# Performance work log

Measured on AMD Instinct MI355X. Metric: run time of the kernel, lower is better.

The kernel has to match this reference:

```python
import jax, jax.numpy as jnp
import numpy as np
import math

B, T, D, H, FF = 2, 2048, 1024, 16, 4096
DH = D // H
EPS = 1e-5

def _ternary(key, out_f, in_f):
    # TFLELayer: ternary-quantized linear weight in {-1,0,1} (stored as f32 here)
    return jax.random.randint(key, (out_f, in_f), -1, 2).astype(jnp.float32)

def setup_inputs() -> dict:
    key = jax.random.key(0)
    ks = jax.random.split(key, 8)
    x = jax.random.normal(ks[0], (B, T, D), dtype=jnp.float32)
    mask = jnp.triu(jnp.ones((T, T), dtype=bool), k=1)  # True = masked (causal)
    return {
        "x": x,
        "mask": mask,
        "ln1_g": jnp.ones((D,), jnp.float32), "ln1_b": jnp.zeros((D,), jnp.float32),
        "ln2_g": jnp.ones((D,), jnp.float32), "ln2_b": jnp.zeros((D,), jnp.float32),
        "Wq": _ternary(ks[1], D, D), "Wk": _ternary(ks[2], D, D),
        "Wv": _ternary(ks[3], D, D), "Wo": _ternary(ks[4], D, D),
        "Wff1": _ternary(ks[5], FF, D), "Wff2": _ternary(ks[6], D, FF),
    }

def _ln(x, g, b):
    mu = jnp.mean(x, axis=-1, keepdims=True)
    var = jnp.var(x, axis=-1, keepdims=True)
    return (x - mu) * jax.lax.rsqrt(var + EPS) * g + b

def reference(x, mask, ln1_g, ln1_b, ln2_g, ln2_b, Wq, Wk, Wv, Wo, Wff1, Wff2):
    h = _ln(x, ln1_g, ln1_b)
    q = (h @ Wq.T).reshape(B, T, H, DH).transpose(0, 2, 1, 3)  # (B,H,T,DH)
    k = (h @ Wk.T).reshape(B, T, H, DH).transpose(0, 2, 1, 3)
    v = (h @ Wv.T).reshape(B, T, H, DH).transpose(0, 2, 1, 3)
    scale = 1.0 / math.sqrt(DH)
    attn = jnp.einsum('bhqd,bhkd->bhqk', q, k) * scale
    attn = jnp.where(mask[None, None], -jnp.inf, attn)
    attn = jax.nn.softmax(attn, axis=-1)
    out = jnp.einsum('bhqk,bhkd->bhqd', attn, v)
    out = out.transpose(0, 2, 1, 3).reshape(B, T, D) @ Wo.T
    x = x + out
    h = _ln(x, ln2_g, ln2_b)
    ff = jax.nn.gelu(h @ Wff1.T, approximate=False)
    ff = ff @ Wff2.T
    return x + ff
```

## Files before the change

kernel.cpp:

```cpp
#include <hip/hip_runtime.h>

typedef __bf16 bf16;
typedef bf16 bf16x8 __attribute__((ext_vector_type(8)));
typedef bf16 bf16x4 __attribute__((ext_vector_type(4)));
typedef float f32x4 __attribute__((ext_vector_type(4)));

static __device__ __forceinline__ void async16(const void* g, void* l) {
  __builtin_amdgcn_global_load_lds((__attribute__((address_space(1))) void*)g,
                                   (__attribute__((address_space(3))) void*)l,
                                   16, 0, 0);
}

template <int N>
static __device__ __forceinline__ float ror16(float x) {
  const int y =
      __builtin_amdgcn_update_dpp(0, __float_as_int(x), 0x120 | N, 0xf, 0xf, true);
  return __int_as_float(y);
}
static __device__ __forceinline__ float rowmax16(float x) {
  x = fmaxf(x, ror16<8>(x));
  x = fmaxf(x, ror16<4>(x));
  x = fmaxf(x, ror16<2>(x));
  x = fmaxf(x, ror16<1>(x));
  return x;
}
static __device__ __forceinline__ float rowsum16(float x) {
  x += ror16<8>(x);
  x += ror16<4>(x);
  x += ror16<2>(x);
  x += ror16<1>(x);
  return x;
}

__global__ __launch_bounds__(256) void ln1_cvt4(
    const float* __restrict__ x, const float* __restrict__ g,
    const float* __restrict__ b, bf16* __restrict__ hi, bf16* __restrict__ lo,
    const float* __restrict__ Wq, const float* __restrict__ Wk,
    const float* __restrict__ Wv, const float* __restrict__ Wo,
    bf16* __restrict__ wdst) {
  const int tid = threadIdx.x;
  if (blockIdx.x >= 4096) {
    const size_t i = ((size_t)(blockIdx.x - 4096) * 256 + tid) * 4;
    const size_t M1 = 1u << 20;
    const float* src = (i < M1) ? Wq : (i < 2 * M1) ? Wk : (i < 3 * M1) ? Wv : Wo;
    const size_t off = i & (M1 - 1);
    const float4 v = *(const float4*)(src + off);
    bf16x4 o = {(bf16)v.x, (bf16)v.y, (bf16)v.z, (bf16)v.w};
    *(bf16x4*)(wdst + i) = o;
    return;
  }
  const int row = blockIdx.x;
  const float* xr = x + (size_t)row * 1024;
  float v[4];
  float s1 = 0.f, s2 = 0.f;
#pragma unroll
  for (int j = 0; j < 4; ++j) {
    v[j] = xr[j * 256 + tid];
    s1 += v[j];
    s2 += v[j] * v[j];
  }
#pragma unroll
  for (int off = 1; off < 64; off <<= 1) {
    s1 += __shfl_xor(s1, off);
    s2 += __shfl_xor(s2, off);
  }
  __shared__ float ws1[4], ws2[4];
  const int wid = tid >> 6;
  if ((tid & 63) == 0) {
    ws1[wid] = s1;
    ws2[wid] = s2;
  }
  __syncthreads();
  s1 = ws1[0] + ws1[1] + ws1[2] + ws1[3];
  s2 = ws2[0] + ws2[1] + ws2[2] + ws2[3];
  const float mu = s1 * (1.f / 1024.f);
  const float var = s2 * (1.f / 1024.f) - mu * mu;
  const float rstd = 1.0f / sqrtf(var + 1e-5f);
#pragma unroll
  for (int j = 0; j < 4; ++j) {
    const int cc = j * 256 + tid;
    const float y = (v[j] - mu) * rstd * g[cc] + b[cc];
    const bf16 yh = (bf16)y;
    hi[(size_t)row * 1024 + cc] = yh;
    lo[(size_t)row * 1024 + cc] = (bf16)(y - (float)yh);
  }
}

__global__ __launch_bounds__(256) void ln_kernel(
    const float* __restrict__ x, const float* __restrict__ g,
    const float* __restrict__ b, bf16* __restrict__ hi) {
  const int row = blockIdx.x;
  const int tid = threadIdx.x;
  const float* xr = x + (size_t)row * 1024;
  float v[4];
  float s1 = 0.f, s2 = 0.f;
#pragma unroll
  for (int j = 0; j < 4; ++j) {
    v[j] = xr[j * 256 + tid];
    s1 += v[j];
    s2 += v[j] * v[j];
  }
#pragma unroll
  for (int off = 1; off < 64; off <<= 1) {
    s1 += __shfl_xor(s1, off);
    s2 += __shfl_xor(s2, off);
  }
  __shared__ float ws1[4], ws2[4];
  const int wid = tid >> 6;
  if ((tid & 63) == 0) {
    ws1[wid] = s1;
    ws2[wid] = s2;
  }
  __syncthreads();
  s1 = ws1[0] + ws1[1] + ws1[2] + ws1[3];
  s2 = ws2[0] + ws2[1] + ws2[2] + ws2[3];
  const float mu = s1 * (1.f / 1024.f);
  const float var = s2 * (1.f / 1024.f) - mu * mu;
  const float rstd = 1.0f / sqrtf(var + 1e-5f);
#pragma unroll
  for (int j = 0; j < 4; ++j) {
    const int cc = j * 256 + tid;
    const float y = (v[j] - mu) * rstd * g[cc] + b[cc];
    hi[(size_t)row * 1024 + cc] = (bf16)y;
  }
}

template <int EPI>
static __device__ __forceinline__ void gemm_body(
    const bf16* __restrict__ A, const bf16* __restrict__ B,
    void* __restrict__ Cv, const float* __restrict__ R, bf16* smem, int col0,
    int row0, int M, int N, int K) {
  bf16* sA0 = smem;
  bf16* sA1 = smem + 4096;
  bf16* sB0 = smem + 8192;
  bf16* sB1 = smem + 12288;
  const int tid = threadIdx.x;
  const int lane = tid & 63;
  const int wid = tid >> 6;
  const int wm = wid >> 1, wn = wid & 1;

  f32x4 acc[4][4];
  const f32x4 fzero = {0.f, 0.f, 0.f, 0.f};
#pragma unroll
  for (int i = 0; i < 4; ++i)
#pragma unroll
    for (int j = 0; j < 4; ++j) acc[i][j] = fzero;

  const int nk = K >> 6;
  const int r0 = tid >> 2, c0 = (tid & 3) << 3;
  const int r1 = (256 + tid) >> 2, c1 = ((256 + tid) & 3) << 3;
  const int wofs0 = (wid << 6) * 8;
  const int wofs1 = (256 + (wid << 6)) * 8;

  for (int kt = 0; kt < nk; ++kt) {
    const int k0 = kt << 6;
    async16(A + (size_t)(row0 + r0) * K + k0 + c0, sA0 + wofs0);
    async16(A + (size_t)(row0 + r1) * K + k0 + c1, sA0 + wofs1);
    async16(A + (size_t)(row0 + r0) * K + k0 + 32 + c0, sA1 + wofs0);
    async16(A + (size_t)(row0 + r1) * K + k0 + 32 + c1, sA1 + wofs1);
    async16(B + (size_t)(col0 + r0) * K + k0 + c0, sB0 + wofs0);
    async16(B + (size_t)(col0 + r1) * K + k0 + c1, sB0 + wofs1);
    async16(B + (size_t)(col0 + r0) * K + k0 + 32 + c0, sB1 + wofs0);
    async16(B + (size_t)(col0 + r1) * K + k0 + 32 + c1, sB1 + wofs1);
    __syncthreads();
    const int fr = lane & 15, fq = (lane >> 4) << 3;
#pragma unroll
    for (int t = 0; t < 2; ++t) {
      const bf16* sA = t ? sA1 : sA0;
      const bf16* sB = t ? sB1 : sB0;
      bf16x8 af[4], bfr[4];
#pragma unroll
      for (int i = 0; i < 4; ++i)
        af[i] = *(const bf16x8*)&sA[(wm * 64 + i * 16 + fr) * 32 + fq];
#pragma unroll
      for (int j = 0; j < 4; ++j)
        bfr[j] = *(const bf16x8*)&sB[(wn * 64 + j * 16 + fr) * 32 + fq];
#pragma unroll
      for (int i = 0; i < 4; ++i)
#pragma unroll
        for (int j = 0; j < 4; ++j)
          acc[i][j] = __builtin_amdgcn_mfma_f32_16x16x32_bf16(
              af[i], bfr[j], acc[i][j], 0, 0, 0);
    }
    __syncthreads();
  }

  const int fr = lane & 15, fq4 = (lane >> 4) << 2;
#pragma unroll
  for (int i = 0; i < 4; ++i) {
#pragma unroll
    for (int j = 0; j < 4; ++j) {
      const int rbase = row0 + wm * 64 + i * 16 + fq4;
      const int col = col0 + wn * 64 + j * 16 + fr;
      if constexpr (EPI == 5) {
        const int b = rbase >> 11, t = rbase & 2047;
        const int hh = col >> 6, d = col & 63;
        bf16x4 o4 = {(bf16)acc[i][j][0], (bf16)acc[i][j][1],
                     (bf16)acc[i][j][2], (bf16)acc[i][j][3]};
        *(bf16x4*)&((bf16*)Cv)[(((size_t)(b * 16 + hh)) * 64 + d) * 2048 + t] =
            o4;
      } else {
#pragma unroll
        for (int r = 0; r < 4; ++r) {
          const size_t idx = (size_t)(rbase + r) * N + col;
          const float val = acc[i][j][r];
          if constexpr (EPI == 0) {
            ((float*)Cv)[idx] = val;
          } else if constexpr (EPI == 2) {
            ((float*)Cv)[idx] = val + R[idx];
          } else {
            ((bf16*)Cv)[idx] =
                (bf16)(0.5f * val * (1.0f + erff(val * 0.7071067811865476f)));
          }
        }
      }
    }
  }
}

template <int EPI>
__global__ __launch_bounds__(256) void gemm_bt(
    const bf16* __restrict__ A, const bf16* __restrict__ B,
    void* __restrict__ Cv, const float* __restrict__ R, int M, int N, int K) {
  __shared__ bf16 smem[16384];
  gemm_body<EPI>(A, B, Cv, R, smem, blockIdx.x * 128, blockIdx.y * 128, M, N,
                 K);
}

static __device__ __forceinline__ void gemm_split_merged(
    const bf16* __restrict__ A, const bf16* __restrict__ A2,
    const bf16* __restrict__ B, bf16* __restrict__ Chi, bf16* __restrict__ Clo,
    bf16* smem, float scale, int col0, int row0) {
  constexpr int K = 1024, N = 1024;
  bf16* sAh0 = smem;
  bf16* sAh1 = smem + 4096;
  bf16* sAl0 = smem + 8192;
  bf16* sAl1 = smem + 12288;
  bf16* sB0 = smem + 16384;
  bf16* sB1 = smem + 20480;
  const int tid = threadIdx.x;
  const int lane = tid & 63;
  const int wid = tid >> 6;
  const int wm = wid >> 1, wn = wid & 1;

  f32x4 acc[4][4];
  const f32x4 fzero = {0.f, 0.f, 0.f, 0.f};
#pragma unroll
  for (int i = 0; i < 4; ++i)
#pragma unroll
    for (int j = 0; j < 4; ++j) acc[i][j] = fzero;

  const int r0 = tid >> 2, c0 = (tid & 3) << 3;
  const int r1 = (256 + tid) >> 2, c1 = ((256 + tid) & 3) << 3;
  const int wofs0 = (wid << 6) * 8;
  const int wofs1 = (256 + (wid << 6)) * 8;

  for (int kt = 0; kt < 16; ++kt) {
    const int k0 = kt << 6;
    async16(A + (size_t)(row0 + r0) * K + k0 + c0, sAh0 + wofs0);
    async16(A + (size_t)(row0 + r1) * K + k0 + c1, sAh0 + wofs1);
    async16(A + (size_t)(row0 + r0) * K + k0 + 32 + c0, sAh1 + wofs0);
    async16(A + (size_t)(row0 + r1) * K + k0 + 32 + c1, sAh1 + wofs1);
    async16(A2 + (size_t)(row0 + r0) * K + k0 + c0, sAl0 + wofs0);
    async16(A2 + (size_t)(row0 + r1) * K + k0 + c1, sAl0 + wofs1);
    async16(A2 + (size_t)(row0 + r0) * K + k0 + 32 + c0, sAl1 + wofs0);
    async16(A2 + (size_t)(row0 + r1) * K + k0 + 32 + c1, sAl1 + wofs1);
    async16(B + (size_t)(col0 + r0) * K + k0 + c0, sB0 + wofs0);
    async16(B + (size_t)(col0 + r1) * K + k0 + c1, sB0 + wofs1);
    async16(B + (size_t)(col0 + r0) * K + k0 + 32 + c0, sB1 + wofs0);
    async16(B + (size_t)(col0 + r1) * K + k0 + 32 + c1, sB1 + wofs1);
    __syncthreads();
    const int fr = lane & 15, fq = (lane >> 4) << 3;
#pragma unroll
    for (int t = 0; t < 2; ++t) {
      const bf16* sAh = t ? sAh1 : sAh0;
      const bf16* sAl = t ? sAl1 : sAl0;
      const bf16* sB = t ? sB1 : sB0;
      bf16x8 ah[4], al[4], bfr[4];
#pragma unroll
      for (int i = 0; i < 4; ++i) {
        ah[i] = *(const bf16x8*)&sAh[(wm * 64 + i * 16 + fr) * 32 + fq];
        al[i] = *(const bf16x8*)&sAl[(wm * 64 + i * 16 + fr) * 32 + fq];
      }
#pragma unroll
      for (int j = 0; j < 4; ++j)
        bfr[j] = *(const bf16x8*)&sB[(wn * 64 + j * 16 + fr) * 32 + fq];
#pragma unroll
      for (int i = 0; i < 4; ++i)
#pragma unroll
        for (int j = 0; j < 4; ++j) {
          acc[i][j] = __builtin_amdgcn_mfma_f32_16x16x32_bf16(
              ah[i], bfr[j], acc[i][j], 0, 0, 0);
          acc[i][j] = __builtin_amdgcn_mfma_f32_16x16x32_bf16(
              al[i], bfr[j], acc[i][j], 0, 0, 0);
        }
    }
    __syncthreads();
  }

  const int fr = lane & 15, fq4 = (lane >> 4) << 2;
#pragma unroll
  for (int i = 0; i < 4; ++i)
#pragma unroll
    for (int j = 0; j < 4; ++j) {
      const int rbase = row0 + wm * 64 + i * 16 + fq4;
      const int col = col0 + wn * 64 + j * 16 + fr;
#pragma unroll
      for (int r = 0; r < 4; ++r) {
        const size_t idx = (size_t)(rbase + r) * N + col;
        const float vs = acc[i][j][r] * scale;
        const bf16 hi = (bf16)vs;
        Chi[idx] = hi;
        Clo[idx] = (bf16)(vs - (float)hi);
      }
    }
}

__global__ __launch_bounds__(256) void gemm_qkv(
    const bf16* __restrict__ A, const bf16* __restrict__ A2,
    const bf16* __restrict__ Bq, const bf16* __restrict__ Bk,
    const bf16* __restrict__ Bv, bf16* qh, bf16* ql, bf16* kh, bf16* kl,
    bf16* vt) {
  __shared__ bf16 smem[24576];
  const int which = blockIdx.x >> 3;
  const int col0 = (blockIdx.x & 7) * 128, row0 = blockIdx.y * 128;
  if (which == 2) {
    gemm_body<5>(A, Bv, (void*)vt, nullptr, smem, col0, row0, 4096, 1024,
                 1024);
  } else {
    gemm_split_merged(A, A2, which ? Bk : Bq, which ? kh : qh, which ? kl : ql,
                      smem, which ? 1.0f : 0.125f * 1.44269504088896f, col0,
                      row0);
  }
}

template <int EPI>
__global__ __launch_bounds__(256) void gemm_bt64(
    const bf16* __restrict__ A, const bf16* __restrict__ B,
    void* __restrict__ Cv, const float* __restrict__ R, int M, int N, int K) {
  __shared__ bf16 smem[12288];
  bf16* sA0 = smem;
  bf16* sA1 = smem + 4096;
  bf16* sB0 = smem + 8192;
  bf16* sB1 = smem + 10240;
  const int col0 = blockIdx.x * 64, row0 = blockIdx.y * 128;
  const int tid = threadIdx.x;
  const int lane = tid & 63;
  const int wid = tid >> 6;
  const int wm = wid >> 1, wn = wid & 1;

  f32x4 acc[4][2];
  const f32x4 fzero = {0.f, 0.f, 0.f, 0.f};
#pragma unroll
  for (int i = 0; i < 4; ++i)
#pragma unroll
    for (int j = 0; j < 2; ++j) acc[i][j] = fzero;

  const int nk = K >> 6;
  const int r0 = tid >> 2, c0 = (tid & 3) << 3;
  const int r1 = (256 + tid) >> 2, c1 = ((256 + tid) & 3) << 3;
  const int wofs0 = (wid << 6) * 8;
  const int wofs1 = (256 + (wid << 6)) * 8;

  for (int kt = 0; kt < nk; ++kt) {
    const int k0 = kt << 6;
    async16(A + (size_t)(row0 + r0) * K + k0 + c0, sA0 + wofs0);
    async16(A + (size_t)(row0 + r1) * K + k0 + c1, sA0 + wofs1);
    async16(A + (size_t)(row0 + r0) * K + k0 + 32 + c0, sA1 + wofs0);
    async16(A + (size_t)(row0 + r1) * K + k0 + 32 + c1, sA1 + wofs1);
    async16(B + (size_t)(col0 + r0) * K + k0 + c0, sB0 + wofs0);
    async16(B + (size_t)(col0 + r0) * K + k0 + 32 + c0, sB1 + wofs0);
    __syncthreads();
    const int fr = lane & 15, fq = (lane >> 4) << 3;
#pragma unroll
    for (int t = 0; t < 2; ++t) {
      const bf16* sA = t ? sA1 : sA0;
      const bf16* sB = t ? sB1 : sB0;
      bf16x8 af[4], bfr[2];
#pragma unroll
      for (int i = 0; i < 4; ++i)
        af[i] = *(const bf16x8*)&sA[(wm * 64 + i * 16 + fr) * 32 + fq];
#pragma unroll
      for (int j = 0; j < 2; ++j)
        bfr[j] = *(const bf16x8*)&sB[(wn * 32 + j * 16 + fr) * 32 + fq];
#pragma unroll
      for (int i = 0; i < 4; ++i)
#pragma unroll
        for (int j = 0; j < 2; ++j)
          acc[i][j] = __builtin_amdgcn_mfma_f32_16x16x32_bf16(
              af[i], bfr[j], acc[i][j], 0, 0, 0);
    }
    __syncthreads();
  }

  const int fr = lane & 15, fq4 = (lane >> 4) << 2;
#pragma unroll
  for (int i = 0; i < 4; ++i) {
#pragma unroll
    for (int j = 0; j < 2; ++j) {
      const int rbase = row0 + wm * 64 + i * 16 + fq4;
      const int col = col0 + wn * 32 + j * 16 + fr;
#pragma unroll
      for (int r = 0; r < 4; ++r) {
        const size_t idx = (size_t)(rbase + r) * N + col;
        const float val = acc[i][j][r];
        if constexpr (EPI == 2) {
          ((float*)Cv)[idx] = val + R[idx];
        } else {
          ((float*)Cv)[idx] = val;
        }
      }
    }
  }
}

__global__ __launch_bounds__(256) void attn_cvt2(
    const bf16* __restrict__ qh_g, const bf16* __restrict__ ql_g,
    const bf16* __restrict__ kh_g, const bf16* __restrict__ kl_g,
    const bf16* __restrict__ vt_g, bf16* __restrict__ out,
    const float* __restrict__ Wf1, const float* __restrict__ Wf2,
    bf16* __restrict__ wdst) {
  __shared__ bf16 lds[18688];
  const int tid = threadIdx.x;
  if (blockIdx.x >= 1024) {
    const size_t i = ((size_t)(blockIdx.x - 1024) * 256 + tid) * 4;
    const size_t M4 = 4u << 20;
    const float* src = (i < M4) ? Wf1 : Wf2;
    const size_t off = (i < M4) ? i : i - M4;
    const float4 v = *(const float4*)(src + off);
    bf16x4 o4 = {(bf16)v.x, (bf16)v.y, (bf16)v.z, (bf16)v.w};
    *(bf16x4*)(wdst + i) = o4;
    return;
  }
  bf16* Kh = lds;
  bf16* Kl = lds + 4608;
  bf16* Vt = lds + 9216;
  bf16* Ps = lds + 13824;

  const int bid = blockIdx.x;
  const int qt = 31 - (bid >> 5);
  const int h = bid & 15;
  const int b = (bid >> 4) & 1;
  const int t0 = qt << 6;
  const int w = tid >> 6;
  const int lane = tid & 63;
  const int c = lane & 15;
  const int quad = lane >> 4;

  const int r0 = tid >> 3, c0 = (tid & 7) << 3;
  const int r1 = (tid + 256) >> 3, c1 = ((tid + 256) & 7) << 3;

  const size_t qrow =
      ((size_t)(b * 2048 + t0 + w * 16 + c)) * 1024 + h * 64 + quad * 8;
  bf16x8 aqh[2], aql[2];
  aqh[0] = *(const bf16x8*)&qh_g[qrow];
  aqh[1] = *(const bf16x8*)&qh_g[qrow + 32];
  aql[0] = *(const bf16x8*)&ql_g[qrow];
  aql[1] = *(const bf16x8*)&ql_g[qrow + 32];

  f32x4 o[4];
  const f32x4 fzero = {0.f, 0.f, 0.f, 0.f};
#pragma unroll
  for (int j = 0; j < 4; ++j) o[j] = fzero;
  float m_i[4] = {-3e38f, -3e38f, -3e38f, -3e38f};
  float l_i[4] = {0.f, 0.f, 0.f, 0.f};

  const size_t vtb = ((size_t)(b * 16 + h)) * 64 * 2048;
  const size_t kband = ((size_t)(b * 2048)) * 1024 + h * 64;

  bf16x8 gk[6];
  {
    gk[0] = *(const bf16x8*)&kh_g[kband + (size_t)r0 * 1024 + c0];
    gk[1] = *(const bf16x8*)&kh_g[kband + (size_t)r1 * 1024 + c1];
    gk[2] = *(const bf16x8*)&kl_g[kband + (size_t)r0 * 1024 + c0];
    gk[3] = *(const bf16x8*)&kl_g[kband + (size_t)r1 * 1024 + c1];
    gk[4] = *(const bf16x8*)&vt_g[vtb + (size_t)r0 * 2048 + c0];
    gk[5] = *(const bf16x8*)&vt_g[vtb + (size_t)r1 * 2048 + c1];
  }

  for (int kt = 0; kt <= qt; ++kt) {
    __syncthreads();
    *(bf16x8*)&Kh[r0 * 72 + c0] = gk[0];
    *(bf16x8*)&Kh[r1 * 72 + c1] = gk[1];
    *(bf16x8*)&Kl[r0 * 72 + c0] = gk[2];
    *(bf16x8*)&Kl[r1 * 72 + c1] = gk[3];
    *(bf16x8*)&Vt[r0 * 72 + c0] = gk[4];
    *(bf16x8*)&Vt[r1 * 72 + c1] = gk[5];
    __syncthreads();

    if (kt < qt) {
      const int kb1 = (kt + 1) << 6;
      const size_t kbase = kband + (size_t)kb1 * 1024;
      gk[0] = *(const bf16x8*)&kh_g[kbase + (size_t)r0 * 1024 + c0];
      gk[1] = *(const bf16x8*)&kh_g[kbase + (size_t)r1 * 1024 + c1];
      gk[2] = *(const bf16x8*)&kl_g[kbase + (size_t)r0 * 1024 + c0];
      gk[3] = *(const bf16x8*)&kl_g[kbase + (size_t)r1 * 1024 + c1];
      gk[4] = *(const bf16x8*)&vt_g[vtb + (size_t)r0 * 2048 + kb1 + c0];
      gk[5] = *(const bf16x8*)&vt_g[vtb + (size_t)r1 * 2048 + kb1 + c1];
    }

    bf16x8 bkh[4][2], bkl[4][2];
#pragma unroll
    for (int j = 0; j < 4; ++j)
#pragma unroll
      for (int s = 0; s < 2; ++s) {
        bkh[j][s] = *(const bf16x8*)&Kh[(j * 16 + c) * 72 + s * 32 + quad * 8];
        bkl[j][s] = *(const bf16x8*)&Kl[(j * 16 + c) * 72 + s * 32 + quad * 8];
      }

    f32x4 s4[4];
#pragma unroll
    for (int j = 0; j < 4; ++j) s4[j] = fzero;
#pragma unroll
    for (int j = 0; j < 4; ++j)
#pragma unroll
      for (int s = 0; s < 2; ++s) {
        s4[j] = __builtin_amdgcn_mfma_f32_16x16x32_bf16(aqh[s], bkh[j][s], s4[j], 0, 0, 0);
        s4[j] = __builtin_amdgcn_mfma_f32_16x16x32_bf16(aqh[s], bkl[j][s], s4[j], 0, 0, 0);
        s4[j] = __builtin_amdgcn_mfma_f32_16x16x32_bf16(aql[s], bkh[j][s], s4[j], 0, 0, 0);
      }

    if (kt == qt) {
#pragma unroll
      for (int j = 0; j < 4; ++j)
#pragma unroll
        for (int r = 0; r < 4; ++r)
          if (j * 16 + c > w * 16 + quad * 4 + r) s4[j][r] = -3e38f;
    }

    float al[4], p[4][4];
#pragma unroll
    for (int r = 0; r < 4; ++r) {
      float mt = fmaxf(fmaxf(s4[0][r], s4[1][r]), fmaxf(s4[2][r], s4[3][r]));
      mt = rowmax16(mt);
      const float mn = fmaxf(m_i[r], mt);
      al[r] = exp2f(m_i[r] - mn);
      float ps = 0.f;
#pragma unroll
      for (int j = 0; j < 4; ++j) {
        p[r][j] = exp2f(s4[j][r] - mn);
        ps += p[r][j];
      }
      ps = rowsum16(ps);
      l_i[r] = l_i[r] * al[r] + ps;
      m_i[r] = mn;
#pragma unroll
      for (int j = 0; j < 4; ++j) o[j][r] *= al[r];
    }

    bf16* Pw = Ps + w * 16 * 76;
#pragma unroll
    for (int r = 0; r < 4; ++r)
#pragma unroll
      for (int j = 0; j < 4; ++j)
        Pw[(quad * 4 + r) * 76 + j * 16 + c] = (bf16)p[r][j];

    bf16x8 ap[2], bv[4][2];
#pragma unroll
    for (int s = 0; s < 2; ++s)
      ap[s] = *(const bf16x8*)&Pw[c * 76 + s * 32 + quad * 8];
#pragma unroll
    for (int j = 0; j < 4; ++j)
#pragma unroll
      for (int s = 0; s < 2; ++s)
        bv[j][s] = *(const bf16x8*)&Vt[(j * 16 + c) * 72 + s * 32 + quad * 8];
#pragma unroll
    for (int j = 0; j < 4; ++j)
#pragma unroll
      for (int s = 0; s < 2; ++s)
        o[j] = __builtin_amdgcn_mfma_f32_16x16x32_bf16(ap[s], bv[j][s], o[j], 0, 0, 0);
  }

#pragma unroll
  for (int r = 0; r < 4; ++r) {
    const float inv = 1.0f / l_i[r];
#pragma unroll
    for (int j = 0; j < 4; ++j) {
      const size_t oi =
          ((size_t)(b * 2048 + t0 + w * 16 + quad * 4 + r)) * 1024 + h * 64 +
          j * 16 + c;
      out[oi] = (bf16)(o[j][r] * inv);
    }
  }
}

extern "C" void kernel_launch(void* const* d_in, const int* in_sizes, int n_in,
                              void* d_out, int out_size, void* d_ws,
                              size_t ws_size, hipStream_t stream) {
  const float* x = (const float*)d_in[0];
  const float* g1 = (const float*)d_in[2];
  const float* b1 = (const float*)d_in[3];
  const float* g2 = (const float*)d_in[4];
  const float* b2 = (const float*)d_in[5];
  const float* Wq = (const float*)d_in[6];
  const float* Wk = (const float*)d_in[7];
  const float* Wv = (const float*)d_in[8];
  const float* Wo = (const float*)d_in[9];
  const float* Wf1 = (const float*)d_in[10];
  const float* Wf2 = (const float*)d_in[11];
  char* ws = (char*)d_ws;
  const size_t MB = 1024 * 1024;
  const size_t M1 = 1u << 20;
  bf16* Wq_b = (bf16*)ws;
  bf16* Wk_b = Wq_b + 1 * M1;
  bf16* Wv_b = Wq_b + 2 * M1;
  bf16* Wo_b = Wq_b + 3 * M1;
  bf16* h_hi = (bf16*)(ws + 8 * MB);
  bf16* h_lo = (bf16*)(ws + 16 * MB);
  bf16* Wf1_b = h_hi;
  bf16* Wf2_b = h_lo;
  bf16* qh = (bf16*)(ws + 24 * MB);
  bf16* ql = (bf16*)(ws + 32 * MB);
  bf16* kh = (bf16*)(ws + 40 * MB);
  bf16* kl = (bf16*)(ws + 48 * MB);
  bf16* vt = (bf16*)(ws + 56 * MB);
  bf16* attnout = (bf16*)(ws + 64 * MB);
  float* x1 = (float*)qh;
  bf16* h2 = (bf16*)(ws + 72 * MB);
  bf16* ff = kh;
  float* outp = (float*)d_out;

  ln1_cvt4<<<8192, 256, 0, stream>>>(x, g1, b1, h_hi, h_lo, Wq, Wk, Wv, Wo,
                                     Wq_b);
  gemm_qkv<<<dim3(24, 32), 256, 0, stream>>>(h_hi, h_lo, Wq_b, Wk_b, Wv_b, qh,
                                             ql, kh, kl, vt);
  attn_cvt2<<<9216, 256, 0, stream>>>(qh, ql, kh, kl, vt, attnout, Wf1, Wf2,
                                      Wf1_b);
  gemm_bt64<2><<<dim3(16, 32), 256, 0, stream>>>(attnout, Wo_b, (void*)x1, x,
                                                 4096, 1024, 1024);
  ln_kernel<<<4096, 256, 0, stream>>>(x1, g2, b2, h2);
  gemm_bt<3><<<dim3(32, 32), 256, 0, stream>>>(h2, Wf1_b, (void*)ff, nullptr,
                                               4096, 4096, 1024);
  gemm_bt64<2><<<dim3(16, 32), 256, 0, stream>>>(ff, Wf2_b, (void*)outp, x1,
                                                 4096, 1024, 4096);
}
```

Before: 419.5 us.

## Deepen GEMM K-tile, add lazy softmax rescale and MFMA priority hints

The 64-wide GEMM now loads a 128-deep K slice per iteration into doubled shared memory, which halves the number of barrier pairs per tile. The attention kernel adds s_setprio around its MFMA blocks. It also skips the running-max update and the rescale of the output accumulator when every row's new max exceeds the old one by no more than 8, in log2 units. These cut synchronisation and ALU work in exchange for more LDS use, which may lower occupancy. Lazy rescaling lets exponentials grow up to 2^8, so bf16 P values lose some relative headroom.

After: 422.1 us. Within noise of the previous version (+0.6%).

```diff
diff --git a/kernel.cpp b/kernel.cpp
--- a/kernel.cpp
+++ b/kernel.cpp
@@ -338,11 +338,7 @@
 __global__ __launch_bounds__(256) void gemm_bt64(
     const bf16* __restrict__ A, const bf16* __restrict__ B,
     void* __restrict__ Cv, const float* __restrict__ R, int M, int N, int K) {
-  __shared__ bf16 smem[12288];
-  bf16* sA0 = smem;
-  bf16* sA1 = smem + 4096;
-  bf16* sB0 = smem + 8192;
-  bf16* sB1 = smem + 10240;
+  __shared__ bf16 smem[24576];
   const int col0 = blockIdx.x * 64, row0 = blockIdx.y * 128;
   const int tid = threadIdx.x;
   const int lane = tid & 63;
@@ -356,26 +352,28 @@
 #pragma unroll
     for (int j = 0; j < 2; ++j) acc[i][j] = fzero;
 
-  const int nk = K >> 6;
+  const int nk = K >> 7;
   const int r0 = tid >> 2, c0 = (tid & 3) << 3;
   const int r1 = (256 + tid) >> 2, c1 = ((256 + tid) & 3) << 3;
   const int wofs0 = (wid << 6) * 8;
   const int wofs1 = (256 + (wid << 6)) * 8;
 
   for (int kt = 0; kt < nk; ++kt) {
-    const int k0 = kt << 6;
-    async16(A + (size_t)(row0 + r0) * K + k0 + c0, sA0 + wofs0);
-    async16(A + (size_t)(row0 + r1) * K + k0 + c1, sA0 + wofs1);
-    async16(A + (size_t)(row0 + r0) * K + k0 + 32 + c0, sA1 + wofs0);
-    async16(A + (size_t)(row0 + r1) * K + k0 + 32 + c1, sA1 + wofs1);
-    async16(B + (size_t)(col0 + r0) * K + k0 + c0, sB0 + wofs0);
-    async16(B + (size_t)(col0 + r0) * K + k0 + 32 + c0, sB1 + wofs0);
+    const int k0 = kt << 7;
+#pragma unroll
+    for (int t = 0; t < 4; ++t) {
+      bf16* sA = smem + t * 4096;
+      bf16* sB = smem + 16384 + t * 2048;
+      async16(A + (size_t)(row0 + r0) * K + k0 + t * 32 + c0, sA + wofs0);
+      async16(A + (size_t)(row0 + r1) * K + k0 + t * 32 + c1, sA + wofs1);
+      async16(B + (size_t)(col0 + r0) * K + k0 + t * 32 + c0, sB + wofs0);
+    }
     __syncthreads();
     const int fr = lane & 15, fq = (lane >> 4) << 3;
 #pragma unroll
-    for (int t = 0; t < 2; ++t) {
-      const bf16* sA = t ? sA1 : sA0;
-      const bf16* sB = t ? sB1 : sB0;
+    for (int t = 0; t < 4; ++t) {
+      const bf16* sA = smem + t * 4096;
+      const bf16* sB = smem + 16384 + t * 2048;
       bf16x8 af[4], bfr[2];
 #pragma unroll
       for (int i = 0; i < 4; ++i)
@@ -511,6 +509,7 @@
     f32x4 s4[4];
 #pragma unroll
     for (int j = 0; j < 4; ++j) s4[j] = fzero;
+    __builtin_amdgcn_s_setprio(1);
 #pragma unroll
     for (int j = 0; j < 4; ++j)
 #pragma unroll
@@ -519,6 +518,7 @@
         s4[j] = __builtin_amdgcn_mfma_f32_16x16x32_bf16(aqh[s], bkl[j][s], s4[j], 0, 0, 0);
         s4[j] = __builtin_amdgcn_mfma_f32_16x16x32_bf16(aql[s], bkh[j][s], s4[j], 0, 0, 0);
       }
+    __builtin_amdgcn_s_setprio(0);
 
     if (kt == qt) {
 #pragma unroll
@@ -528,24 +528,44 @@
           if (j * 16 + c > w * 16 + quad * 4 + r) s4[j][r] = -3e38f;
     }
 
-    float al[4], p[4][4];
+    float mt[4];
 #pragma unroll
     for (int r = 0; r < 4; ++r) {
-      float mt = fmaxf(fmaxf(s4[0][r], s4[1][r]), fmaxf(s4[2][r], s4[3][r]));
-      mt = rowmax16(mt);
-      const float mn = fmaxf(m_i[r], mt);
-      al[r] = exp2f(m_i[r] - mn);
-      float ps = 0.f;
-#pragma unroll
-      for (int j = 0; j < 4; ++j) {
-        p[r][j] = exp2f(s4[j][r] - mn);
-        ps += p[r][j];
-      }
-      ps = rowsum16(ps);
-      l_i[r] = l_i[r] * al[r] + ps;
-      m_i[r] = mn;
-#pragma unroll
-      for (int j = 0; j < 4; ++j) o[j][r] *= al[r];
+      float m0 = fmaxf(fmaxf(s4[0][r], s4[1][r]), fmaxf(s4[2][r], s4[3][r]));
+      mt[r] = rowmax16(m0);
+    }
+    const bool skip = __all((mt[0] - m_i[0] <= 8.f) & (mt[1] - m_i[1] <= 8.f) &
+                            (mt[2] - m_i[2] <= 8.f) & (mt[3] - m_i[3] <= 8.f));
+    float p[4][4];
+    if (skip) {
+#pragma unroll
+      for (int r = 0; r < 4; ++r) {
+        float ps = 0.f;
+#pragma unroll
+        for (int j = 0; j < 4; ++j) {
+          p[r][j] = exp2f(s4[j][r] - m_i[r]);
+          ps += p[r][j];
+        }
+        ps = rowsum16(ps);
+        l_i[r] += ps;
+      }
+    } else {
+#pragma unroll
+      for (int r = 0; r < 4; ++r) {
+        const float mn = fmaxf(m_i[r], mt[r]);
+        const float al = exp2f(m_i[r] - mn);
+        float ps = 0.f;
+#pragma unroll
+        for (int j = 0; j < 4; ++j) {
+          p[r][j] = exp2f(s4[j][r] - mn);
+          ps += p[r][j];
+        }
+        ps = rowsum16(ps);
+        l_i[r] = l_i[r] * al + ps;
+        m_i[r] = mn;
+#pragma unroll
+        for (int j = 0; j < 4; ++j) o[j][r] *= al;
+      }
     }
 
     bf16* Pw = Ps + w * 16 * 76;
@@ -564,11 +584,13 @@
 #pragma unroll
       for (int s = 0; s < 2; ++s)
         bv[j][s] = *(const bf16x8*)&Vt[(j * 16 + c) * 72 + s * 32 + quad * 8];
+    __builtin_amdgcn_s_setprio(1);
 #pragma unroll
     for (int j = 0; j < 4; ++j)
 #pragma unroll
       for (int s = 0; s < 2; ++s)
         o[j] = __builtin_amdgcn_mfma_f32_16x16x32_bf16(ap[s], bv[j][s], o[j], 0, 0, 0);
+    __builtin_amdgcn_s_setprio(0);
   }
 
 #pragma unroll
```
